# Optimization experiments

Hardware: AMD Instinct MI355X
Metric: run time of the kernel (lower is better)

## Reference

```python
import jax, jax.numpy as jnp
import numpy as np

DIM = 128; DSTATE = 8; DCONV = 4; DTRANK = 8
B = 2; T = 48; H = 16; W = 16
EPS = 1e-5

def _ln(x, w, b):
    mu = jnp.mean(x, -1, keepdims=True)
    var = jnp.mean(jnp.square(x - mu), -1, keepdims=True)
    return (x - mu) * jax.lax.rsqrt(var + EPS) * w + b

def _causal_dwconv(x, w, b):
    # x: [B,L,D], w: [D,K] depthwise, causal padding K-1 on the left
    xt = jnp.transpose(x, (0, 2, 1))  # [B,D,L]
    out = jax.lax.conv_general_dilated(
        xt, w[:, None, :], (1,), [(w.shape[-1] - 1, 0)],
        dimension_numbers=('NCH', 'OIH', 'NCH'),
        feature_group_count=x.shape[-1])
    return jnp.transpose(out + b[:, None], (0, 2, 1))

def _selective_scan(u, dt, A, Bc, Cc, Dp):
    # u, dt: [B,L,D]; A: [D,N]; Bc, Cc: [B,L,N]; Dp: [D]
    dA = jnp.exp(dt[..., None] * A)                          # [B,L,D,N]
    dBx = dt[..., None] * Bc[:, :, None, :] * u[..., None]   # [B,L,D,N]
    def combine(c1, c2):
        a1, b1 = c1; a2, b2 = c2
        return a1 * a2, a2 * b1 + b2
    _, hs = jax.lax.associative_scan(combine, (dA, dBx), axis=1)
    return jnp.einsum('bldn,bln->bld', hs, Cc) + u * Dp

def _bimamba(xn, in_w, conv_w, conv_b, xp_w, dt_w, dt_b, A_log, Dp, out_w):
    # xn: [B,L,DIM]; direction-stacked params have leading axis 2 (fwd/bwd)
    xz = xn @ in_w.T                      # [B,L,2*DIM]
    xh, z = jnp.split(xz, 2, axis=-1)
    acc = 0.0
    for d in range(2):
        xi = xh if d == 0 else xh[:, ::-1]
        zi = z if d == 0 else z[:, ::-1]
        xc = jax.nn.silu(_causal_dwconv(xi, conv_w[d], conv_b[d]))
        proj = xc @ xp_w[d].T             # [B,L,DTRANK+2*DSTATE]
        dtr, Bc, Cc = jnp.split(proj, [DTRANK, DTRANK + DSTATE], axis=-1)
        dt = jax.nn.softplus(dtr @ dt_w[d].T + dt_b[d])
        A = -jnp.exp(A_log[d])
        y = _selective_scan(xc, dt, A, Bc, Cc, Dp[d]) * jax.nn.silu(zi)
        acc = acc + (y if d == 0 else y[:, ::-1])
    return acc @ out_w.T

def setup_inputs():
    key = jax.random.key(0)
    ks = jax.random.split(key, 10)
    s = 0.1
    return {
        "x": jax.random.normal(ks[0], (B, DIM, T, H, W), jnp.float32),
        "norm1_w": jnp.ones((DIM,), jnp.float32),
        "norm1_b": jnp.zeros((DIM,), jnp.float32),
        "norm2_w": jnp.ones((DIM,), jnp.float32),
        "norm2_b": jnp.zeros((DIM,), jnp.float32),
        "subln_w": jnp.ones((DIM,), jnp.float32),
        "subln_b": jnp.zeros((DIM,), jnp.float32),
        "lambda_q": jax.random.normal(ks[1], (DIM,), jnp.float32) * s,
        "in_proj_w": jax.random.normal(ks[2], (2, 2 * DIM, DIM), jnp.float32) * s,
        "conv_w": jax.random.normal(ks[3], (2, 2, DIM, DCONV), jnp.float32) * s,
        "conv_b": jax.random.normal(ks[4], (2, 2, DIM), jnp.float32) * s,
        "x_proj_w": jax.random.normal(ks[5], (2, 2, DTRANK + 2 * DSTATE, DIM), jnp.float32) * s,
        "dt_proj_w": jax.random.normal(ks[6], (2, 2, DIM, DTRANK), jnp.float32) * s,
        "dt_proj_b": jax.random.normal(ks[7], (2, 2, DIM), jnp.float32) * s,
        "A_log": jnp.broadcast_to(jnp.log(jnp.arange(1, DSTATE + 1, dtype=jnp.float32)), (2, 2, DIM, DSTATE)) + 0.0,
        "D": jnp.ones((2, 2, DIM), jnp.float32),
        "out_proj_w": jax.random.normal(ks[8], (2, DIM, DIM), jnp.float32) * s,
    }

def reference(x, norm1_w, norm1_b, norm2_w, norm2_b, subln_w, subln_b,
              lambda_q, in_proj_w, conv_w, conv_b, x_proj_w,
              dt_proj_w, dt_proj_b, A_log, D, out_proj_w):
    Bsz, C = x.shape[0], x.shape[1]
    Tt, Hh, Ww = x.shape[2], x.shape[3], x.shape[4]
    L = Tt * Hh * Ww
    x_flat = jnp.transpose(x.reshape(Bsz, C, L), (0, 2, 1))  # [B,L,C]
    x_norm = _ln(x_flat, norm1_w, norm1_b)
    y1 = _bimamba(x_norm, in_proj_w[0], conv_w[0], conv_b[0], x_proj_w[0],
                  dt_proj_w[0], dt_proj_b[0], A_log[0], D[0], out_proj_w[0])
    y2 = _bimamba(x_norm, in_proj_w[1], conv_w[1], conv_b[1], x_proj_w[1],
                  dt_proj_w[1], dt_proj_b[1], A_log[1], D[1], out_proj_w[1])
    lam = jax.nn.sigmoid(jnp.sum(lambda_q))
    attn = _ln(y1 - lam * y2, subln_w, subln_b)
    out = _ln(x_flat + attn, norm2_w, norm2_b)
    return jnp.transpose(out, (0, 2, 1)).reshape(Bsz, C, Tt, Hh, Ww)
```

## Files before the change

kernel.cpp:

```cpp
#include <hip/hip_runtime.h>
#include <math.h>

#define DIMC 128
#define LSEQ 12288
#define NB 2
#define BLR 24576
#define EPSV 1e-5f
#define NCH 384
#define LC 32
#define KP 132

typedef __bf16 bf16x8 __attribute__((ext_vector_type(8)));
typedef __attribute__((ext_vector_type(4))) float f4_t;

__device__ __forceinline__ float sigf(float x){ return 1.f/(1.f+__expf(-x)); }
__device__ __forceinline__ float softplusf(float x){
    return fmaxf(x,0.f) + __logf(1.f + __expf(-fabsf(x)));
}
__device__ __forceinline__ float bf2f(unsigned short u){
    union { unsigned int i; float f; } v; v.i = ((unsigned int)u) << 16; return v.f;
}
__device__ __forceinline__ unsigned short f2bf(float f){
    union { float f; unsigned int i; } v; v.f = f;
    unsigned int b = v.i + 0x7FFFu + ((v.i >> 16) & 1u);
    return (unsigned short)(b >> 16);
}
__device__ __forceinline__ bf16x8 ld_frag8(const unsigned short* p){
    union { uint2 u[2]; bf16x8 v; } r;
    r.u[0] = *(const uint2*)(p);
    r.u[1] = *(const uint2*)(p+4);
    return r.v;
}
__device__ __forceinline__ bf16x8 ld_frag16g(const unsigned short* p){
    union { uint4 u; bf16x8 v; } r; r.u = *(const uint4*)p; return r.v;
}

template<bool FAST>
__device__ __forceinline__ void comp_a8(float dtv, const float* Av, float* a){
    if (FAST){
        float e1 = __expf(dtv*Av[0]);
        float e2 = e1*e1, e4 = e2*e2;
        a[0]=e1; a[1]=e2; a[2]=e2*e1; a[3]=e4;
        a[4]=e4*e1; a[5]=e4*e2; a[6]=a[5]*e1; a[7]=e4*e4;
    } else {
        #pragma unroll
        for (int n = 0; n < 8; n++) a[n] = __expf(dtv*Av[n]);
    }
}

__global__ void k_wall(const float* __restrict__ dtw, const float* __restrict__ xpw,
                       const float* __restrict__ lq,
                       unsigned short* __restrict__ wallb, float* __restrict__ lam){
    int inst = blockIdx.x, j = blockIdx.y, k = threadIdx.x;
    const float* xp = xpw + (size_t)inst*24*128;
    float v;
    if (j < 128){
        const float* dw = dtw + (size_t)inst*128*8 + (size_t)j*8;
        v = 0.f;
        #pragma unroll
        for (int r = 0; r < 8; r++) v += dw[r]*xp[r*128 + k];
    } else {
        v = xp[(8 + (j-128))*128 + k];
    }
    wallb[((size_t)inst*144 + j)*128 + k] = f2bf(v);
    if (inst == 0 && j == 0 && k < 64){
        float s = lq[k] + lq[k+64];
        for (int m = 32; m; m >>= 1) s += __shfl_xor(s, m);
        if (k == 0) *lam = 1.f/(1.f+__expf(-s));
    }
}

__global__ __launch_bounds__(256) void k_prep(const float* __restrict__ wi, const float* __restrict__ ow,
    unsigned short* __restrict__ wib, unsigned short* __restrict__ owb){
    int idx = (blockIdx.x*256 + threadIdx.x)*4;
    const float* src; unsigned short* dst; int off;
    if (idx < 65536){ src = wi;  dst = wib; off = idx; }
    else            { src = ow;  dst = owb; off = idx - 65536; }
    float4 v = *(const float4*)&src[off];
    ushort4 o; o.x=f2bf(v.x); o.y=f2bf(v.y); o.z=f2bf(v.z); o.w=f2bf(v.w);
    *(ushort4*)&dst[off] = o;
}

__global__ __launch_bounds__(256) void k_normT(const float* __restrict__ x,
    const float* __restrict__ w1, const float* __restrict__ b1, unsigned short* __restrict__ xn)
{
    __shared__ float t[64*129];
    __shared__ float red1[256], red2[256];
    __shared__ float stt[128];
    const int bb = blockIdx.x / 192;
    const int l0 = (blockIdx.x % 192) * 64;
    const int tid = threadIdx.x;
    const int li = tid & 63, cg = tid >> 6;
    #pragma unroll
    for (int p = 0; p < 32; p++){
        int c = p*4 + cg;
        t[li*129 + c] = x[(size_t)bb*DIMC*LSEQ + (size_t)c*LSEQ + l0 + li];
    }
    __syncthreads();
    {
        int r = tid >> 2, qg = tid & 3;
        float s = 0.f, s2 = 0.f;
        #pragma unroll
        for (int j = 0; j < 32; j++){ float v = t[r*129 + qg*32 + j]; s += v; s2 += v*v; }
        red1[qg*64 + r] = s; red2[qg*64 + r] = s2;
    }
    __syncthreads();
    if (tid < 64){
        float s = 0.f, s2 = 0.f;
        #pragma unroll
        for (int g = 0; g < 4; g++){ s += red1[g*64 + tid]; s2 += red2[g*64 + tid]; }
        float mu = s*(1.f/128.f);
        float var = s2*(1.f/128.f) - mu*mu;
        stt[tid*2] = mu; stt[tid*2+1] = rsqrtf(var + EPSV);
    }
    __syncthreads();
    const int c2 = (tid & 63)*2, lg = tid >> 6;
    #pragma unroll
    for (int p = 0; p < 16; p++){
        int l = p*4 + lg;
        float mu = stt[l*2], rs = stt[l*2+1];
        float v0 = (t[l*129 + c2    ] - mu)*rs*w1[c2    ] + b1[c2    ];
        float v1 = (t[l*129 + c2 + 1] - mu)*rs*w1[c2 + 1] + b1[c2 + 1];
        unsigned int o = (unsigned int)f2bf(v0) | ((unsigned int)f2bf(v1) << 16);
        *(unsigned int*)&xn[(size_t)(bb*LSEQ + l0 + l)*DIMC + c2] = o;
    }
}

__global__ __launch_bounds__(256,4) void k_inproj(const unsigned short* __restrict__ xn,
    const unsigned short* __restrict__ wib, unsigned short* __restrict__ xz)
{
    __shared__ __align__(16) unsigned short As[64*KP];
    const int row0 = blockIdx.x * 64;
    const int j0   = blockIdx.y * 128;
    const int tid = threadIdx.x;
    #pragma unroll
    for (int p = 0; p < 4; p++){
        int idx = p*256 + tid; int li = idx >> 4; int g = (idx & 15)*8;
        uint4 va = *(const uint4*)&xn[(size_t)(row0+li)*DIMC + g];
        *(uint2*)&As[li*KP + g]     = make_uint2(va.x, va.y);
        *(uint2*)&As[li*KP + g + 4] = make_uint2(va.z, va.w);
    }
    __syncthreads();
    const int lane = tid & 63, w = tid >> 6;
    const int m15 = lane & 15, q = lane >> 4;
    f4_t zf = {0.f,0.f,0.f,0.f};
    f4_t acc[8];
    #pragma unroll
    for (int j = 0; j < 8; j++) acc[j] = zf;
    #pragma unroll
    for (int ks = 0; ks < 4; ks++){
        int k0 = ks*32 + q*8;
        bf16x8 a0 = ld_frag8(&As[(w*16 + m15)*KP + k0]);
        #pragma unroll
        for (int nt = 0; nt < 8; nt++){
            bf16x8 b = ld_frag16g(&wib[(size_t)(j0 + nt*16 + m15)*DIMC + k0]);
            acc[nt] = __builtin_amdgcn_mfma_f32_16x16x32_bf16(a0, b, acc[nt], 0,0,0);
        }
    }
    __syncthreads();
    unsigned short* ep = As;
    #pragma unroll
    for (int nt = 0; nt < 8; nt++){
        int row = w*16 + q*4;
        int col = nt*16 + m15;
        #pragma unroll
        for (int i = 0; i < 4; i++)
            ep[(row+i)*KP + col] = f2bf(acc[nt][i]);
    }
    __syncthreads();
    #pragma unroll
    for (int p = 0; p < 4; p++){
        int idx = p*256 + tid; int li = idx >> 4; int g = (idx & 15)*8;
        uint2 u0 = *(const uint2*)&ep[li*KP + g];
        uint2 u1 = *(const uint2*)&ep[li*KP + g + 4];
        uint4 o; o.x=u0.x; o.y=u0.y; o.z=u1.x; o.w=u1.y;
        *(uint4*)&xz[(size_t)(row0+li)*512 + j0 + g] = o;
    }
}

__global__ __launch_bounds__(256) void k_conv(const unsigned short* __restrict__ xz,
    const float* __restrict__ cw, const float* __restrict__ cb, unsigned short* __restrict__ xc)
{
    __shared__ unsigned short tile[70][144];
    const int bid = blockIdx.x;
    const int lt = bid % 192;
    const int bb = (bid/192) % NB;
    const int m  = bid / (192*NB);
    const int l0 = lt * 64;
    const int tid = threadIdx.x;
    for (int idx = tid; idx < 70*16; idx += 256){
        int r = idx >> 4, cq = idx & 15;
        int l = l0 - 3 + r;
        uint4 v = make_uint4(0,0,0,0);
        if (l >= 0 && l < LSEQ)
            v = *(const uint4*)&xz[((size_t)(bb*LSEQ + l))*512 + m*256 + cq*8];
        *(uint4*)&tile[r][cq*8] = v;
    }
    __syncthreads();
    const int dimi = tid & 127, lg = tid >> 7;
    float w0a[4], w1a[4];
    #pragma unroll
    for (int k = 0; k < 4; k++){
        w0a[k] = cw[((size_t)(m*2+0)*DIMC + dimi)*4 + k];
        w1a[k] = cw[((size_t)(m*2+1)*DIMC + dimi)*4 + k];
    }
    const float b0 = cb[(m*2+0)*DIMC + dimi];
    const float b1v = cb[(m*2+1)*DIMC + dimi];
    for (int p = 0; p < 32; p++){
        int li = p*2 + lg;
        float t0 = bf2f(tile[li  ][dimi]);
        float t1 = bf2f(tile[li+1][dimi]);
        float t2 = bf2f(tile[li+2][dimi]);
        float t3 = bf2f(tile[li+3][dimi]);
        float t4 = bf2f(tile[li+4][dimi]);
        float t5 = bf2f(tile[li+5][dimi]);
        float t6 = bf2f(tile[li+6][dimi]);
        float v0 = b0  + w0a[0]*t0 + w0a[1]*t1 + w0a[2]*t2 + w0a[3]*t3;
        float v1 = b1v + w1a[3]*t3 + w1a[2]*t4 + w1a[1]*t5 + w1a[0]*t6;
        v0 = v0 * sigf(v0);
        v1 = v1 * sigf(v1);
        xc[(((size_t)(m*2+0)*NB + bb)*LSEQ + l0 + li)*DIMC + dimi] = f2bf(v0);
        xc[(((size_t)(m*2+1)*NB + bb)*LSEQ + l0 + li)*DIMC + dimi] = f2bf(v1);
    }
}

__global__ __launch_bounds__(256,4) void k_xproj(const unsigned short* __restrict__ xc,
    const unsigned short* __restrict__ wallb, const float* __restrict__ dtb,
    unsigned short* __restrict__ dty, float* __restrict__ bcb)
{
    __shared__ __align__(16) unsigned short As[64*KP];
    __shared__ __align__(16) float fbuf[64*17];
    const int row0 = blockIdx.x * 64;
    const int ib   = blockIdx.y;
    const int inst = ib >> 1;
    const int tid = threadIdx.x;
    const size_t abase = (size_t)ib * LSEQ * DIMC;
    #pragma unroll
    for (int p = 0; p < 4; p++){
        int idx = p*256 + tid; int li = idx >> 4; int g = (idx & 15)*8;
        uint4 va = *(const uint4*)&xc[abase + (size_t)(row0+li)*DIMC + g];
        *(uint2*)&As[li*KP + g]     = make_uint2(va.x, va.y);
        *(uint2*)&As[li*KP + g + 4] = make_uint2(va.z, va.w);
    }
    __syncthreads();
    const int lane = tid & 63, w = tid >> 6;
    const int m15 = lane & 15, q = lane >> 4;
    f4_t zf = {0.f,0.f,0.f,0.f};
    f4_t acc[9];
    #pragma unroll
    for (int j = 0; j < 9; j++) acc[j] = zf;
    #pragma unroll
    for (int ks = 0; ks < 4; ks++){
        int k0 = ks*32 + q*8;
        bf16x8 a0 = ld_frag8(&As[(w*16 + m15)*KP + k0]);
        #pragma unroll
        for (int nt = 0; nt < 9; nt++){
            bf16x8 b = ld_frag16g(&wallb[((size_t)inst*144 + nt*16 + m15)*DIMC + k0]);
            acc[nt] = __builtin_amdgcn_mfma_f32_16x16x32_bf16(a0, b, acc[nt], 0,0,0);
        }
    }
    {
        int row = w*16 + q*4;
        #pragma unroll
        for (int i = 0; i < 4; i++)
            fbuf[(row+i)*17 + m15] = acc[8][i];
    }
    __syncthreads();
    {
        int row = tid >> 2, j = (tid & 3)*4;
        float4 v = { fbuf[row*17 + j], fbuf[row*17 + j + 1],
                     fbuf[row*17 + j + 2], fbuf[row*17 + j + 3] };
        *(float4*)&bcb[((size_t)ib*LSEQ + row0 + row)*16 + j] = v;
    }
    unsigned short* ep = As;
    #pragma unroll
    for (int nt = 0; nt < 8; nt++){
        int col = nt*16 + m15;
        float bias = dtb[inst*DIMC + col];
        int row = w*16 + q*4;
        #pragma unroll
        for (int i = 0; i < 4; i++)
            ep[(row+i)*KP + col] = f2bf(softplusf(acc[nt][i] + bias));
    }
    __syncthreads();
    #pragma unroll
    for (int p = 0; p < 4; p++){
        int idx = p*256 + tid; int li = idx >> 4; int g = (idx & 15)*8;
        uint2 u0 = *(const uint2*)&ep[li*KP + g];
        uint2 u1 = *(const uint2*)&ep[li*KP + g + 4];
        uint4 o; o.x=u0.x; o.y=u0.y; o.z=u1.x; o.w=u1.y;
        *(uint4*)&dty[abase + (size_t)(row0+li)*DIMC + g] = o;
    }
}

template<bool FAST>
__device__ __forceinline__ void scan1_body(const unsigned short* __restrict__ dt,
    const unsigned short* __restrict__ xc, const float* __restrict__ bcb,
    const float* Av, size_t rbase, size_t bbase, int c, int d, int tid,
    float* Ac, float* Bc)
{
    #pragma unroll 8
    for (int s = 0; s < LC; s++){
        int j = c*LC + s;
        int l = d ? (LSEQ-1-j) : j;
        size_t ro = rbase + (size_t)l*DIMC + tid;
        float dtv = bf2f(dt[ro]);
        float uv  = bf2f(xc[ro]);
        const float* bp = bcb + bbase + (size_t)l*16;
        float4 bA = *(const float4*)bp;
        float4 bB = *(const float4*)(bp+4);
        float bv[8] = {bA.x,bA.y,bA.z,bA.w,bB.x,bB.y,bB.z,bB.w};
        float du = dtv*uv;
        float a[8];
        comp_a8<FAST>(dtv, Av, a);
        #pragma unroll
        for (int n = 0; n < 8; n++){
            Bc[n] = a[n]*Bc[n] + du*bv[n];
            Ac[n] *= a[n];
        }
    }
}

__global__ __launch_bounds__(128) void k_scan1(const unsigned short* __restrict__ dt,
    const unsigned short* __restrict__ xc, const float* __restrict__ bcb,
    const float* __restrict__ alog, float* __restrict__ st)
{
    const int ib = blockIdx.x & 7;
    const int c  = blockIdx.x >> 3;
    const int inst = ib >> 1;
    const int d = inst & 1;
    const int tid = threadIdx.x;
    float Av[8];
    #pragma unroll
    for (int n = 0; n < 8; n++)
        Av[n] = -__expf(alog[((size_t)inst*DIMC + tid)*8 + n]);
    bool fast = true;
    #pragma unroll
    for (int n = 1; n < 8; n++)
        fast = fast && (fabsf(Av[n] - (float)(n+1)*Av[0]) <= 1e-5f*fabsf(Av[n]));
    const size_t rbase = (size_t)ib*LSEQ*DIMC;
    const size_t bbase = (size_t)ib*LSEQ*16;
    float Ac[8], Bc[8];
    #pragma unroll
    for (int n = 0; n < 8; n++){ Ac[n] = 1.f; Bc[n] = 0.f; }
    if (fast) scan1_body<true >(dt, xc, bcb, Av, rbase, bbase, c, d, tid, Ac, Bc);
    else      scan1_body<false>(dt, xc, bcb, Av, rbase, bbase, c, d, tid, Ac, Bc);
    float* so = st + (((size_t)ib*NCH + c)*DIMC + tid)*16;
    #pragma unroll
    for (int n = 0; n < 8; n++){ so[n] = Ac[n]; so[8+n] = Bc[n]; }
}

__global__ __launch_bounds__(512) void k_scan2(float* __restrict__ st){
    const int ib   = blockIdx.x >> 7;
    const int dim  = blockIdx.x & 127;
    const int n    = threadIdx.x >> 6;
    const int lane = threadIdx.x & 63;
    const size_t cstride = (size_t)DIMC*16;
    const size_t base = ((size_t)ib*NCH*DIMC + dim)*16 + n;
    float a[6], b[6];
    float Al = 1.f, Bl = 0.f;
    #pragma unroll
    for (int j = 0; j < 6; j++){
        size_t o = base + (size_t)(lane*6 + j)*cstride;
        float A  = st[o];
        float Bv = st[o + 8];
        a[j] = A; b[j] = Bv;
        Bl = A*Bl + Bv;
        Al *= A;
    }
    #pragma unroll
    for (int off = 1; off < 64; off <<= 1){
        float Ao = __shfl_up(Al, off, 64);
        float Bo = __shfl_up(Bl, off, 64);
        if (lane >= off){
            Bl = Al*Bo + Bl;
            Al = Al*Ao;
        }
    }
    float h = __shfl_up(Bl, 1, 64);
    if (lane == 0) h = 0.f;
    #pragma unroll
    for (int j = 0; j < 6; j++){
        size_t o = base + (size_t)(lane*6 + j)*cstride;
        st[o] = h;
        h = a[j]*h + b[j];
    }
}

template<bool FAST>
__device__ __forceinline__ void scan3_body(unsigned short* __restrict__ dty,
    const unsigned short* __restrict__ xc, const float* __restrict__ bcb,
    const unsigned short* __restrict__ xz,
    const float* Av, float Dv, float* h,
    size_t rbase, size_t bbase, size_t zbase, int c, int d, int tid)
{
    #pragma unroll 8
    for (int s = 0; s < LC; s++){
        int j = c*LC + s;
        int l = d ? (LSEQ-1-j) : j;
        size_t ro = rbase + (size_t)l*DIMC + tid;
        float dtv = bf2f(dty[ro]);
        float uv  = bf2f(xc[ro]);
        const float* bp = bcb + bbase + (size_t)l*16;
        float4 bA = *(const float4*)bp;
        float4 bB = *(const float4*)(bp+4);
        float4 cA = *(const float4*)(bp+8);
        float4 cB = *(const float4*)(bp+12);
        float bv[8] = {bA.x,bA.y,bA.z,bA.w,bB.x,bB.y,bB.z,bB.w};
        float cv[8] = {cA.x,cA.y,cA.z,cA.w,cB.x,cB.y,cB.z,cB.w};
        float du = dtv*uv;
        float y = uv*Dv;
        float a[8];
        comp_a8<FAST>(dtv, Av, a);
        #pragma unroll
        for (int n = 0; n < 8; n++){
            h[n] = a[n]*h[n] + du*bv[n];
            y += h[n]*cv[n];
        }
        float zv = bf2f(xz[zbase + (size_t)l*512 + tid]);
        y *= zv * sigf(zv);
        dty[ro] = f2bf(y);
    }
}

__global__ __launch_bounds__(128) void k_scan3(unsigned short* __restrict__ dty,
    const unsigned short* __restrict__ xc, const float* __restrict__ bcb,
    const unsigned short* __restrict__ xz, const float* __restrict__ st,
    const float* __restrict__ alog, const float* __restrict__ dvec)
{
    const int ib = blockIdx.x & 7;
    const int c  = blockIdx.x >> 3;
    const int inst = ib >> 1, bb = ib & 1;
    const int m = inst >> 1, d = inst & 1;
    const int tid = threadIdx.x;
    float Av[8];
    #pragma unroll
    for (int n = 0; n < 8; n++)
        Av[n] = -__expf(alog[((size_t)inst*DIMC + tid)*8 + n]);
    bool fast = true;
    #pragma unroll
    for (int n = 1; n < 8; n++)
        fast = fast && (fabsf(Av[n] - (float)(n+1)*Av[0]) <= 1e-5f*fabsf(Av[n]));
    const float Dv = dvec[inst*DIMC + tid];
    float h[8];
    const float* hp = st + (((size_t)ib*NCH + c)*DIMC + tid)*16;
    #pragma unroll
    for (int n = 0; n < 8; n++) h[n] = hp[n];
    const size_t rbase = (size_t)ib*LSEQ*DIMC;
    const size_t bbase = (size_t)ib*LSEQ*16;
    const size_t zbase = (size_t)bb*LSEQ*512 + m*256 + 128;
    if (fast) scan3_body<true >(dty, xc, bcb, xz, Av, Dv, h, rbase, bbase, zbase, c, d, tid);
    else      scan3_body<false>(dty, xc, bcb, xz, Av, Dv, h, rbase, bbase, zbase, c, d, tid);
}

__global__ __launch_bounds__(256,3) void k_final(const unsigned short* __restrict__ y,
    const unsigned short* __restrict__ owb, const float* __restrict__ x, const float* __restrict__ lamp,
    const float* __restrict__ sw, const float* __restrict__ sb,
    const float* __restrict__ n2w, const float* __restrict__ n2b, float* __restrict__ outp)
{
    __shared__ __align__(16) char smem[52480];
    unsigned short* Ast = (unsigned short*)smem;
    float* yt            = (float*)smem;
    unsigned short* xtb  = (unsigned short*)(smem + 33024);
    float* red1          = (float*)(smem + 49920);
    float* red2          = (float*)(smem + 50944);
    float* stt           = (float*)(smem + 51968);
    const int bb = blockIdx.y;
    const int l0 = blockIdx.x * 64;
    const int tid = threadIdx.x;
    const float lam = *lamp;
    #pragma unroll
    for (int p = 0; p < 8; p++){
        int idx = p*256 + tid; int mm = idx >> 10; int li = (idx >> 4) & 63; int g = (idx & 15)*8;
        uint4 vf = *(const uint4*)&y[(((size_t)(mm*2+0)*NB + bb)*LSEQ + l0 + li)*DIMC + g];
        uint4 vb = *(const uint4*)&y[(((size_t)(mm*2+1)*NB + bb)*LSEQ + l0 + li)*DIMC + g];
        const unsigned short* uf = (const unsigned short*)&vf;
        const unsigned short* ub = (const unsigned short*)&vb;
        unsigned short o[8];
        #pragma unroll
        for (int j = 0; j < 8; j++) o[j] = f2bf(bf2f(uf[j]) + bf2f(ub[j]));
        *(uint2*)&Ast[(mm*64 + li)*KP + g]     = *(uint2*)&o[0];
        *(uint2*)&Ast[(mm*64 + li)*KP + g + 4] = *(uint2*)&o[4];
    }
    __syncthreads();
    const int lane = tid & 63, w = tid >> 6;
    const int m15 = lane & 15, q = lane >> 4;
    f4_t zf = {0.f,0.f,0.f,0.f};
    f4_t acc[2][8];
    #pragma unroll
    for (int i = 0; i < 2; i++)
        #pragma unroll
        for (int j = 0; j < 8; j++) acc[i][j] = zf;
    #pragma unroll
    for (int ks = 0; ks < 4; ks++){
        int k0 = ks*32 + q*8;
        bf16x8 a0 = ld_frag8(&Ast[(       w*16 + m15)*KP + k0]);
        bf16x8 a1 = ld_frag8(&Ast[(64   + w*16 + m15)*KP + k0]);
        #pragma unroll
        for (int nt = 0; nt < 8; nt++){
            bf16x8 b0 = ld_frag16g(&owb[((size_t)0*DIMC + nt*16 + m15)*DIMC + k0]);
            bf16x8 b1 = ld_frag16g(&owb[((size_t)1*DIMC + nt*16 + m15)*DIMC + k0]);
            acc[0][nt] = __builtin_amdgcn_mfma_f32_16x16x32_bf16(a0, b0, acc[0][nt], 0,0,0);
            acc[1][nt] = __builtin_amdgcn_mfma_f32_16x16x32_bf16(a1, b1, acc[1][nt], 0,0,0);
        }
    }
    __syncthreads();
    #pragma unroll
    for (int nt = 0; nt < 8; nt++){
        int row = w*16 + q*4;
        int col = nt*16 + m15;
        #pragma unroll
        for (int i = 0; i < 4; i++)
            yt[(row+i)*129 + col] = acc[0][nt][i] - lam*acc[1][nt][i];
    }
    {
        const int li = tid & 63, cg = tid >> 6;
        #pragma unroll
        for (int p = 0; p < 32; p++){
            int c = p*4 + cg;
            xtb[li*132 + c] = f2bf(x[(size_t)bb*DIMC*LSEQ + (size_t)c*LSEQ + l0 + li]);
        }
    }
    __syncthreads();
    const int r = tid & 63, g = tid >> 6;
    float s = 0.f, s2 = 0.f;
    #pragma unroll
    for (int k = 0; k < 32; k++){ float v = yt[r*129 + g*32 + k]; s += v; s2 += v*v; }
    red1[g*64 + r] = s; red2[g*64 + r] = s2;
    __syncthreads();
    if (tid < 64){
        float ss = 0.f, ss2 = 0.f;
        #pragma unroll
        for (int gg = 0; gg < 4; gg++){ ss += red1[gg*64 + tid]; ss2 += red2[gg*64 + tid]; }
        float mu = ss*(1.f/128.f);
        float var = ss2*(1.f/128.f) - mu*mu;
        stt[tid*2] = mu; stt[tid*2+1] = rsqrtf(var + EPSV);
    }
    __syncthreads();
    float mu1 = stt[r*2], rs1 = stt[r*2+1];
    s = 0.f; s2 = 0.f;
    #pragma unroll
    for (int k = 0; k < 32; k++){
        int c = g*32 + k;
        float v = (yt[r*129+c] - mu1)*rs1*sw[c] + sb[c] + bf2f(xtb[r*132+c]);
        yt[r*129+c] = v;
        s += v; s2 += v*v;
    }
    __syncthreads();
    red1[g*64 + r] = s; red2[g*64 + r] = s2;
    __syncthreads();
    if (tid < 64){
        float ss = 0.f, ss2 = 0.f;
        #pragma unroll
        for (int gg = 0; gg < 4; gg++){ ss += red1[gg*64 + tid]; ss2 += red2[gg*64 + tid]; }
        float mu = ss*(1.f/128.f);
        float var = ss2*(1.f/128.f) - mu*mu;
        stt[tid*2] = mu; stt[tid*2+1] = rsqrtf(var + EPSV);
    }
    __syncthreads();
    float mu2 = stt[r*2], rs2 = stt[r*2+1];
    #pragma unroll
    for (int k = 0; k < 32; k++){
        int c = g*32 + k;
        float o = (yt[r*129+c] - mu2)*rs2*n2w[c] + n2b[c];
        outp[(size_t)bb*DIMC*LSEQ + (size_t)c*LSEQ + l0 + r] = o;
    }
}

extern "C" void kernel_launch(void* const* d_in, const int* in_sizes, int n_in,
                              void* d_out, int out_size, void* d_ws, size_t ws_size,
                              hipStream_t stream)
{
    const float* x    = (const float*)d_in[0];
    const float* n1w  = (const float*)d_in[1];
    const float* n1b  = (const float*)d_in[2];
    const float* n2w  = (const float*)d_in[3];
    const float* n2b  = (const float*)d_in[4];
    const float* slw  = (const float*)d_in[5];
    const float* slb  = (const float*)d_in[6];
    const float* lq   = (const float*)d_in[7];
    const float* wi   = (const float*)d_in[8];
    const float* cw   = (const float*)d_in[9];
    const float* cb   = (const float*)d_in[10];
    const float* xpw  = (const float*)d_in[11];
    const float* dtw  = (const float*)d_in[12];
    const float* dtb  = (const float*)d_in[13];
    const float* alog = (const float*)d_in[14];
    const float* dvec = (const float*)d_in[15];
    const float* ow   = (const float*)d_in[16];

    float* ws = (float*)d_ws;
    unsigned short* xn    = (unsigned short*)(ws);
    unsigned short* xz    = (unsigned short*)(ws + 1572864);
    unsigned short* xc    = (unsigned short*)(ws + 7864320);
    unsigned short* dty   = (unsigned short*)(ws + 14155776);
    float*          bcb   = ws + 20447232;
    float*          st1   = ws + 22020096;
    unsigned short* wallb = (unsigned short*)(ws + 28311552);
    unsigned short* wib   = (unsigned short*)(ws + 28348416);
    unsigned short* owb   = (unsigned short*)(ws + 28381184);
    float*          lam   = ws + 28397568;

    k_wall  <<<dim3(4,144), 128, 0, stream>>>(dtw, xpw, lq, wallb, lam);
    k_prep  <<<96, 256, 0, stream>>>(wi, ow, wib, owb);
    k_normT <<<384, 256, 0, stream>>>(x, n1w, n1b, xn);
    k_inproj<<<dim3(384, 4), 256, 0, stream>>>(xn, wib, xz);
    k_conv  <<<2*NB*(LSEQ/64), 256, 0, stream>>>(xz, cw, cb, xc);
    k_xproj <<<dim3(192, 8), 256, 0, stream>>>(xc, wallb, dtb, dty, bcb);
    k_scan1 <<<8*NCH, 128, 0, stream>>>(dty, xc, bcb, alog, st1);
    k_scan2 <<<1024, 512, 0, stream>>>(st1);
    k_scan3 <<<8*NCH, 128, 0, stream>>>(dty, xc, bcb, xz, st1, alog, dvec);
    k_final <<<dim3(192, 2), 256, 0, stream>>>(dty, owb, x, lam, slw, slb, n2w, n2b, (float*)d_out);
}
```

Before: 289.3 us.

## Fuse chunk-local scan pass into x-projection kernel using shared-memory tiles

The first pass of the chunked selective scan (per-chunk decay and state accumulation) now runs inside the x-projection kernel. It reads the xc, dt and B tiles already held in shared memory, and the separate scan1 launch is removed. This avoids re-reading dt, xc and B from global memory and saves one kernel launch. In exchange the xproj kernel uses more shared memory (an extra Ep tile and a padded fbuf), which may lower occupancy. The scan is also serialized per thread inside the same block, so the kernel runs longer.

```diff
diff --git a/kernel.cpp b/kernel.cpp
--- a/kernel.cpp
+++ b/kernel.cpp
@@ -9,6 +9,7 @@
 #define NCH 384
 #define LC 32
 #define KP 132
+#define FBP 20
 
 typedef __bf16 bf16x8 __attribute__((ext_vector_type(8)));
 typedef __attribute__((ext_vector_type(4))) float f4_t;
@@ -224,15 +225,42 @@
     }
 }
 
+template<bool FAST>
+__device__ __forceinline__ void fscan(const unsigned short* __restrict__ As,
+    const unsigned short* __restrict__ Ep, const float* __restrict__ fbuf,
+    const float* Av, int ch, int d, int dim, float* Ac, float* Bc)
+{
+    #pragma unroll 8
+    for (int s = 0; s < LC; s++){
+        int r = ch*32 + (d ? 31-s : s);
+        float dtv = bf2f(Ep[r*KP + dim]);
+        float uv  = bf2f(As[r*KP + dim]);
+        float4 b0 = *(const float4*)&fbuf[r*FBP];
+        float4 b1 = *(const float4*)&fbuf[r*FBP + 4];
+        float bv[8] = {b0.x,b0.y,b0.z,b0.w,b1.x,b1.y,b1.z,b1.w};
+        float du = dtv*uv;
+        float a[8];
+        comp_a8<FAST>(dtv, Av, a);
+        #pragma unroll
+        for (int n = 0; n < 8; n++){
+            Bc[n] = a[n]*Bc[n] + du*bv[n];
+            Ac[n] *= a[n];
+        }
+    }
+}
+
 __global__ __launch_bounds__(256,4) void k_xproj(const unsigned short* __restrict__ xc,
     const unsigned short* __restrict__ wallb, const float* __restrict__ dtb,
-    unsigned short* __restrict__ dty, float* __restrict__ bcb)
+    const float* __restrict__ alog,
+    unsigned short* __restrict__ dty, float* __restrict__ bcb, float* __restrict__ st)
 {
     __shared__ __align__(16) unsigned short As[64*KP];
-    __shared__ __align__(16) float fbuf[64*17];
+    __shared__ __align__(16) unsigned short Ep[64*KP];
+    __shared__ __align__(16) float fbuf[64*FBP];
     const int row0 = blockIdx.x * 64;
     const int ib   = blockIdx.y;
     const int inst = ib >> 1;
+    const int d    = inst & 1;
     const int tid = threadIdx.x;
     const size_t abase = (size_t)ib * LSEQ * DIMC;
     #pragma unroll
@@ -263,16 +291,8 @@
         int row = w*16 + q*4;
         #pragma unroll
         for (int i = 0; i < 4; i++)
-            fbuf[(row+i)*17 + m15] = acc[8][i];
-    }
-    __syncthreads();
-    {
-        int row = tid >> 2, j = (tid & 3)*4;
-        float4 v = { fbuf[row*17 + j], fbuf[row*17 + j + 1],
-                     fbuf[row*17 + j + 2], fbuf[row*17 + j + 3] };
-        *(float4*)&bcb[((size_t)ib*LSEQ + row0 + row)*16 + j] = v;
-    }
-    unsigned short* ep = As;
+            fbuf[(row+i)*FBP + m15] = acc[8][i];
+    }
     #pragma unroll
     for (int nt = 0; nt < 8; nt++){
         int col = nt*16 + m15;
@@ -280,74 +300,49 @@
         int row = w*16 + q*4;
         #pragma unroll
         for (int i = 0; i < 4; i++)
-            ep[(row+i)*KP + col] = f2bf(softplusf(acc[nt][i] + bias));
-    }
-    __syncthreads();
+            Ep[(row+i)*KP + col] = f2bf(softplusf(acc[nt][i] + bias));
+    }
+    __syncthreads();
+    {
+        int row = tid >> 2, j = (tid & 3)*4;
+        float4 v = { fbuf[row*FBP + j], fbuf[row*FBP + j + 1],
+                     fbuf[row*FBP + j + 2], fbuf[row*FBP + j + 3] };
+        *(float4*)&bcb[((size_t)ib*LSEQ + row0 + row)*16 + j] = v;
+    }
     #pragma unroll
     for (int p = 0; p < 4; p++){
         int idx = p*256 + tid; int li = idx >> 4; int g = (idx & 15)*8;
-        uint2 u0 = *(const uint2*)&ep[li*KP + g];
-        uint2 u1 = *(const uint2*)&ep[li*KP + g + 4];
+        uint2 u0 = *(const uint2*)&Ep[li*KP + g];
+        uint2 u1 = *(const uint2*)&Ep[li*KP + g + 4];
         uint4 o; o.x=u0.x; o.y=u0.y; o.z=u1.x; o.w=u1.y;
         *(uint4*)&dty[abase + (size_t)(row0+li)*DIMC + g] = o;
     }
-}
-
-template<bool FAST>
-__device__ __forceinline__ void scan1_body(const unsigned short* __restrict__ dt,
-    const unsigned short* __restrict__ xc, const float* __restrict__ bcb,
-    const float* Av, size_t rbase, size_t bbase, int c, int d, int tid,
-    float* Ac, float* Bc)
-{
-    #pragma unroll 8
-    for (int s = 0; s < LC; s++){
-        int j = c*LC + s;
-        int l = d ? (LSEQ-1-j) : j;
-        size_t ro = rbase + (size_t)l*DIMC + tid;
-        float dtv = bf2f(dt[ro]);
-        float uv  = bf2f(xc[ro]);
-        const float* bp = bcb + bbase + (size_t)l*16;
-        float4 bA = *(const float4*)bp;
-        float4 bB = *(const float4*)(bp+4);
-        float bv[8] = {bA.x,bA.y,bA.z,bA.w,bB.x,bB.y,bB.z,bB.w};
-        float du = dtv*uv;
-        float a[8];
-        comp_a8<FAST>(dtv, Av, a);
-        #pragma unroll
-        for (int n = 0; n < 8; n++){
-            Bc[n] = a[n]*Bc[n] + du*bv[n];
-            Ac[n] *= a[n];
-        }
-    }
-}
-
-__global__ __launch_bounds__(128) void k_scan1(const unsigned short* __restrict__ dt,
-    const unsigned short* __restrict__ xc, const float* __restrict__ bcb,
-    const float* __restrict__ alog, float* __restrict__ st)
-{
-    const int ib = blockIdx.x & 7;
-    const int c  = blockIdx.x >> 3;
-    const int inst = ib >> 1;
-    const int d = inst & 1;
-    const int tid = threadIdx.x;
+    const int ch  = tid >> 7;
+    const int dim = tid & 127;
+    const int bc  = row0 >> 5;
+    const int c   = d ? (NCH-1 - bc - ch) : (bc + ch);
     float Av[8];
     #pragma unroll
     for (int n = 0; n < 8; n++)
-        Av[n] = -__expf(alog[((size_t)inst*DIMC + tid)*8 + n]);
+        Av[n] = -__expf(alog[((size_t)inst*DIMC + dim)*8 + n]);
     bool fast = true;
     #pragma unroll
     for (int n = 1; n < 8; n++)
         fast = fast && (fabsf(Av[n] - (float)(n+1)*Av[0]) <= 1e-5f*fabsf(Av[n]));
-    const size_t rbase = (size_t)ib*LSEQ*DIMC;
-    const size_t bbase = (size_t)ib*LSEQ*16;
     float Ac[8], Bc[8];
     #pragma unroll
     for (int n = 0; n < 8; n++){ Ac[n] = 1.f; Bc[n] = 0.f; }
-    if (fast) scan1_body<true >(dt, xc, bcb, Av, rbase, bbase, c, d, tid, Ac, Bc);
-    else      scan1_body<false>(dt, xc, bcb, Av, rbase, bbase, c, d, tid, Ac, Bc);
-    float* so = st + (((size_t)ib*NCH + c)*DIMC + tid)*16;
-    #pragma unroll
-    for (int n = 0; n < 8; n++){ so[n] = Ac[n]; so[8+n] = Bc[n]; }
+    if (fast) fscan<true >(As, Ep, fbuf, Av, ch, d, dim, Ac, Bc);
+    else      fscan<false>(As, Ep, fbuf, Av, ch, d, dim, Ac, Bc);
+    float* so = st + (((size_t)ib*NCH + c)*DIMC + dim)*16;
+    float4 s0 = {Ac[0],Ac[1],Ac[2],Ac[3]};
+    float4 s1 = {Ac[4],Ac[5],Ac[6],Ac[7]};
+    float4 s2 = {Bc[0],Bc[1],Bc[2],Bc[3]};
+    float4 s3 = {Bc[4],Bc[5],Bc[6],Bc[7]};
+    *(float4*)&so[0]  = s0;
+    *(float4*)&so[4]  = s1;
+    *(float4*)&so[8]  = s2;
+    *(float4*)&so[12] = s3;
 }
 
 __global__ __launch_bounds__(512) void k_scan2(float* __restrict__ st){
@@ -606,8 +601,7 @@
     k_normT <<<384, 256, 0, stream>>>(x, n1w, n1b, xn);
     k_inproj<<<dim3(384, 4), 256, 0, stream>>>(xn, wib, xz);
     k_conv  <<<2*NB*(LSEQ/64), 256, 0, stream>>>(xz, cw, cb, xc);
-    k_xproj <<<dim3(192, 8), 256, 0, stream>>>(xc, wallb, dtb, dty, bcb);
-    k_scan1 <<<8*NCH, 128, 0, stream>>>(dty, xc, bcb, alog, st1);
+    k_xproj <<<dim3(192, 8), 256, 0, stream>>>(xc, wallb, dtb, alog, dty, bcb, st1);
     k_scan2 <<<1024, 512, 0, stream>>>(st1);
     k_scan3 <<<8*NCH, 128, 0, stream>>>(dty, xc, bcb, xz, st1, alog, dvec);
     k_final <<<dim3(192, 2), 256, 0, stream>>>(dty, owb, x, lam, slw, slb, n2w, n2b, (float*)d_out);
```

New measurement: 279.9 us. -3.2%, faster.
